# Optimization experiments

Hardware: AMD Instinct MI355X
Metric: run time of the kernel (lower is better)

Reference implementation:

```python
import jax, jax.numpy as jnp
import numpy as np

N = 100000   # n_nodes
E = 600000   # n_edges
D = 128      # cfg_node_encoding_dim
L = 4        # nr_layers
EPS = 1e-5


def setup_inputs() -> dict:
    key = jax.random.key(0)
    k0, k1, k2, k3 = jax.random.split(key, 4)
    x = jax.random.normal(k0, (N, D), dtype=jnp.float32)
    edge_index = jax.random.randint(k1, (2, E), 0, N, dtype=jnp.int32)
    W = jax.random.normal(k2, (L, D, D), dtype=jnp.float32) * (1.0 / np.sqrt(D))
    b = jax.random.normal(k3, (L, D), dtype=jnp.float32) * 0.01
    gamma = jnp.ones((L, D), dtype=jnp.float32)
    beta = jnp.zeros((L, D), dtype=jnp.float32)
    return {"x": x, "W": W, "b": b, "gamma": gamma, "beta": beta,
            "edge_index": edge_index}


def _gcn_layer(x, W, b, src_sl, dst_sl, norm):
    # PyG GCNConv: h = x @ W, then symmetric-normalized aggregation + bias
    h = x @ W                                  # [N, D]
    msg = h[src_sl] * norm[:, None]            # [E+N, D] gather + scale
    out = jax.ops.segment_sum(msg, dst_sl, num_segments=N)  # scatter-add
    return out + b


def _layer_norm(x, gamma, beta):
    mu = jnp.mean(x, axis=-1, keepdims=True)
    var = jnp.mean(jnp.square(x - mu), axis=-1, keepdims=True)
    return (x - mu) * jax.lax.rsqrt(var + EPS) * gamma + beta


def reference(x, W, b, gamma, beta, edge_index):
    src, dst = edge_index[0], edge_index[1]
    loops = jnp.arange(N, dtype=edge_index.dtype)
    src_sl = jnp.concatenate([src, loops])     # add_self_loops=True
    dst_sl = jnp.concatenate([dst, loops])
    deg = jax.ops.segment_sum(jnp.ones(E + N, dtype=x.dtype), dst_sl,
                              num_segments=N)
    dinv = jnp.where(deg > 0, jax.lax.rsqrt(deg), 0.0)
    norm = dinv[src_sl] * dinv[dst_sl]         # D^{-1/2} (A+I) D^{-1/2}
    h = x
    for i in range(L):
        h = _gcn_layer(h, W[i], b[i], src_sl, dst_sl, norm)
        h = jax.nn.relu(h)
        # dropout is identity in eval mode
        h = _layer_norm(h, gamma[i], beta[i])
    return h
```

## Files before the change

kernel.cpp:

```cpp
#include <hip/hip_runtime.h>
#include <hip/hip_bf16.h>

#define D_DIM 128
#define AST 136
#define CST 132

typedef __attribute__((ext_vector_type(8))) short short8v;
typedef __attribute__((ext_vector_type(4))) short short4v;
typedef __attribute__((ext_vector_type(4))) float floatx4;

__device__ __forceinline__ short f2bf(float x) {
    unsigned u = __builtin_bit_cast(unsigned, x);
    unsigned r = u + 0x7fff + ((u >> 16) & 1);
    return (short)(r >> 16);
}
__device__ __forceinline__ float bflo(unsigned p) {
    return __builtin_bit_cast(float, p << 16);
}
__device__ __forceinline__ float bfhi(unsigned p) {
    return __builtin_bit_cast(float, p & 0xffff0000u);
}


__global__ void zero_cnt_kernel(int* __restrict__ cnt, int n) {
    int i = blockIdx.x * blockDim.x + threadIdx.x;
    if (i < n) cnt[i] = 0;
}

__global__ void count_kernel(const int* __restrict__ dst, int* __restrict__ cnt, int e) {
    int i = blockIdx.x * blockDim.x + threadIdx.x;
    if (i < e) atomicAdd(&cnt[dst[i]], 1);
}

__global__ __launch_bounds__(256) void partial_kernel(const int* __restrict__ cnt,
                                                      int* __restrict__ partial, int n) {
    const int b = blockIdx.x, t = threadIdx.x;
    const int base = b * 1024 + t * 4;
    int s = 0;
    if (base + 3 < n) {
        int4 c = *(const int4*)(cnt + base);
        s = c.x + c.y + c.z + c.w;
    } else {
        for (int j = 0; j < 4; ++j) if (base + j < n) s += cnt[base + j];
    }
    #pragma unroll
    for (int m = 1; m < 64; m <<= 1) s += __shfl_xor(s, m, 64);
    __shared__ int ws[4];
    if ((t & 63) == 0) ws[t >> 6] = s;
    __syncthreads();
    if (t == 0) partial[b] = ws[0] + ws[1] + ws[2] + ws[3];
}

__global__ __launch_bounds__(1024) void scan_partials_kernel(int* __restrict__ partial, int nb,
                                                             int* __restrict__ row_ptr,
                                                             int n, int e) {
    __shared__ int sh[1024];
    const int t = threadIdx.x;
    sh[t] = (t < nb) ? partial[t] : 0;
    __syncthreads();
    for (int off = 1; off < 1024; off <<= 1) {
        int v = (t >= off) ? sh[t - off] : 0;
        __syncthreads();
        sh[t] += v;
        __syncthreads();
    }
    if (t < nb) partial[t] = (t == 0) ? 0 : sh[t - 1];
    if (t == 0) row_ptr[n] = e;
}

__global__ __launch_bounds__(256) void emit_kernel(const int* __restrict__ cnt,
                                                   const int* __restrict__ partial,
                                                   int* __restrict__ row_ptr,
                                                   int* __restrict__ cursor,
                                                   float* __restrict__ dinv, int n) {
    const int b = blockIdx.x, t = threadIdx.x;
    const int base = b * 1024 + t * 4;
    int4 c = make_int4(0, 0, 0, 0);
    if (base + 3 < n) {
        c = *(const int4*)(cnt + base);
    } else {
        if (base     < n) c.x = cnt[base];
        if (base + 1 < n) c.y = cnt[base + 1];
        if (base + 2 < n) c.z = cnt[base + 2];
        if (base + 3 < n) c.w = cnt[base + 3];
    }
    const int ts = c.x + c.y + c.z + c.w;
    int incl = ts;
    const int lane = t & 63;
    #pragma unroll
    for (int off = 1; off < 64; off <<= 1) {
        int v = __shfl_up(incl, off, 64);
        if (lane >= off) incl += v;
    }
    __shared__ int wsum[4];
    if (lane == 63) wsum[t >> 6] = incl;
    __syncthreads();
    const int w = t >> 6;
    int waveoff = 0;
    #pragma unroll
    for (int i = 0; i < 3; ++i) if (i < w) waveoff += wsum[i];
    const int basev = partial[b] + waveoff + (incl - ts);
    const int e0 = basev, e1 = e0 + c.x, e2 = e1 + c.y, e3 = e2 + c.z;
    if (base + 3 < n) {
        *(int4*)(row_ptr + base) = make_int4(e0, e1, e2, e3);
        *(int4*)(cursor  + base) = make_int4(e0, e1, e2, e3);
        *(float4*)(dinv + base) = make_float4(rsqrtf((float)(c.x + 1)), rsqrtf((float)(c.y + 1)),
                                              rsqrtf((float)(c.z + 1)), rsqrtf((float)(c.w + 1)));
    } else {
        int es[4] = {e0, e1, e2, e3};
        int cs[4] = {c.x, c.y, c.z, c.w};
        for (int j = 0; j < 4; ++j) if (base + j < n) {
            row_ptr[base + j] = es[j];
            cursor[base + j]  = es[j];
            dinv[base + j]    = rsqrtf((float)(cs[j] + 1));
        }
    }
}

__global__ void fill_kernel(const int* __restrict__ src, const int* __restrict__ dst,
                            const float* __restrict__ dinv,
                            int* __restrict__ cursor, int2* __restrict__ meta, int e) {
    int i = blockIdx.x * blockDim.x + threadIdx.x;
    if (i < e) {
        int s = src[i], d = dst[i];
        int p = atomicAdd(&cursor[d], 1);
        float w = dinv[s] * dinv[d];
        meta[p] = make_int2(s, __builtin_bit_cast(int, w));
    }
}

__global__ __launch_bounds__(256) void wt_prep_kernel(const float* __restrict__ W,
                                                      short* __restrict__ Wt, int total) {
    int o = blockIdx.x * blockDim.x + threadIdx.x;
    if (o >= total) return;
    int l = o >> 14;
    int r = o & 16383;
    int nn = r >> 7;
    int k  = r & 127;
    Wt[o] = f2bf(W[(size_t)l * 16384 + (size_t)k * 128 + nn]);
}

template <bool IN_F32>
__global__ __launch_bounds__(256) void gemm_mfma_kernel(const void* __restrict__ Xv,
                                                        const short* __restrict__ Wt,
                                                        short* __restrict__ H, int n) {
    __shared__ short Alds[64 * AST];
    const int t    = threadIdx.x;
    const int wv   = t >> 6;
    const int lane = t & 63;
    const int m    = lane & 15;
    const int quad = lane >> 4;
    const int row0 = blockIdx.x * 64;

    short8v bfr[2][4];
    #pragma unroll
    for (int c = 0; c < 2; ++c) {
        const short* bp = Wt + (size_t)((wv * 2 + c) * 16 + m) * D_DIM + quad * 8;
        #pragma unroll
        for (int kt = 0; kt < 4; ++kt)
            bfr[c][kt] = *(const short8v*)(bp + kt * 32);
    }

    if constexpr (IN_F32) {
        const float* X = (const float*)Xv;
        #pragma unroll
        for (int i = 0; i < 8; ++i) {
            int q  = t + i * 256;
            int r  = q >> 5;
            int k4 = q & 31;
            int row = row0 + r;
            float4 v = make_float4(0.f, 0.f, 0.f, 0.f);
            if (row < n) v = *(const float4*)(X + (size_t)row * D_DIM + k4 * 4);
            short4v s;
            s.x = f2bf(v.x); s.y = f2bf(v.y); s.z = f2bf(v.z); s.w = f2bf(v.w);
            *(short4v*)(&Alds[r * AST + k4 * 4]) = s;
        }
    } else {
        const short* X = (const short*)Xv;
        #pragma unroll
        for (int i = 0; i < 4; ++i) {
            int q  = t + i * 256;
            int r  = q >> 4;
            int kc = q & 15;
            int row = row0 + r;
            short8v v = {0,0,0,0,0,0,0,0};
            if (row < n) v = *(const short8v*)(X + (size_t)row * D_DIM + kc * 8);
            *(short8v*)(&Alds[r * AST + kc * 8]) = v;
        }
    }
    __syncthreads();

    floatx4 acc[4][2];
    #pragma unroll
    for (int rt = 0; rt < 4; ++rt) {
        const short* ab = &Alds[(rt * 16 + m) * AST + quad * 8];
        short8v afr[4];
        #pragma unroll
        for (int kt = 0; kt < 4; ++kt) afr[kt] = *(const short8v*)(ab + kt * 32);

        #pragma unroll
        for (int c = 0; c < 2; ++c) {
            floatx4 a = (floatx4){0.f, 0.f, 0.f, 0.f};
            #pragma unroll
            for (int kt = 0; kt < 4; ++kt)
                a = __builtin_amdgcn_mfma_f32_16x16x32_bf16(afr[kt], bfr[c][kt], a, 0, 0, 0);
            acc[rt][c] = a;
        }
    }
    __syncthreads();

    #pragma unroll
    for (int rt = 0; rt < 4; ++rt) {
        #pragma unroll
        for (int c = 0; c < 2; ++c) {
            const int col = (wv * 2 + c) * 16 + m;
            #pragma unroll
            for (int r = 0; r < 4; ++r)
                Alds[(rt * 16 + quad * 4 + r) * CST + col] = f2bf(acc[rt][c][r]);
        }
    }
    __syncthreads();

    #pragma unroll
    for (int i = 0; i < 4; ++i) {
        int q  = t + i * 256;
        int r  = q >> 4;
        int kc = q & 15;
        int row = row0 + r;
        if (row < n)
            *(short8v*)(H + (size_t)row * D_DIM + kc * 8) = *(const short8v*)(&Alds[r * CST + kc * 8]);
    }
}

template <bool OUT_BF16>
__global__ __launch_bounds__(256) void agg_kernel(const short* __restrict__ Hb,
                                                  const int* __restrict__ row_ptr,
                                                  const int2* __restrict__ meta,
                                                  const float* __restrict__ dinv,
                                                  const float* __restrict__ bias,
                                                  const float* __restrict__ gamma,
                                                  const float* __restrict__ beta,
                                                  void* __restrict__ Yv, int n) {
    const int wave = __builtin_amdgcn_readfirstlane(threadIdx.x >> 6);
    const int lane = threadIdx.x & 63;
    const int vA = (blockIdx.x * 4 + wave) * 2;
    if (vA >= n) return;
    const bool hasB = (vA + 1) < n;
    const int vB = hasB ? vA + 1 : vA;

    const float dvA = dinv[vA];
    const float dvB = dinv[vB];
    const int begA = row_ptr[vA];
    const int endA = row_ptr[vA + 1];
    const int begB = row_ptr[vB];
    const int endB = row_ptr[vB + 1];
    const int cntA = endA - begA;
    const int cntB = hasB ? (endB - begB) : 0;
    const int mx = cntA > cntB ? cntA : cntB;

    const unsigned psA = ((const unsigned*)(Hb + (size_t)vA * D_DIM))[lane];
    const unsigned psB = ((const unsigned*)(Hb + (size_t)vB * D_DIM))[lane];
    float axA = bflo(psA) * (dvA * dvA);
    float ayA = bfhi(psA) * (dvA * dvA);
    float axB = bflo(psB) * (dvB * dvB);
    float ayB = bfhi(psB) * (dvB * dvB);

    for (int k = 0; k < mx; k += 4) {
        int   idx[8];
        float wgt[8];
        #pragma unroll
        for (int j = 0; j < 4; ++j) {
            int ii = min(begA + k + j, endA - 1); ii = max(ii, 0);
            const int2 mm = meta[ii];
            idx[j] = mm.x;
            wgt[j] = (k + j < cntA) ? __builtin_bit_cast(float, mm.y) : 0.f;
        }
        #pragma unroll
        for (int j = 0; j < 4; ++j) {
            int ii = min(begB + k + j, endB - 1); ii = max(ii, 0);
            const int2 mm = meta[ii];
            idx[4 + j] = mm.x;
            wgt[4 + j] = (k + j < cntB) ? __builtin_bit_cast(float, mm.y) : 0.f;
        }
        unsigned p[8];
        #pragma unroll
        for (int j = 0; j < 8; ++j)
            p[j] = ((const unsigned*)(Hb + (size_t)idx[j] * D_DIM))[lane];
        #pragma unroll
        for (int j = 0; j < 4; ++j) {
            axA = fmaf(wgt[j], bflo(p[j]), axA);
            ayA = fmaf(wgt[j], bfhi(p[j]), ayA);
            axB = fmaf(wgt[4 + j], bflo(p[4 + j]), axB);
            ayB = fmaf(wgt[4 + j], bfhi(p[4 + j]), ayB);
        }
    }

    const float2 bb = ((const float2*)bias)[lane];
    const float2 gg = ((const float2*)gamma)[lane];
    const float2 be = ((const float2*)beta)[lane];

    #pragma unroll
    for (int s = 0; s < 2; ++s) {
        if (s == 1 && !hasB) break;
        float a0 = fmaxf((s ? axB : axA) + bb.x, 0.f);
        float a1 = fmaxf((s ? ayB : ayA) + bb.y, 0.f);
        float s1 = a0 + a1;
        float s2 = a0 * a0 + a1 * a1;
        #pragma unroll
        for (int m = 1; m < 64; m <<= 1) {
            s1 += __shfl_xor(s1, m, 64);
            s2 += __shfl_xor(s2, m, 64);
        }
        const float mu  = s1 * (1.f / 128.f);
        const float var = s2 * (1.f / 128.f) - mu * mu;
        const float rs  = rsqrtf(var + 1e-5f);
        const float o0 = (a0 - mu) * rs * gg.x + be.x;
        const float o1 = (a1 - mu) * rs * gg.y + be.y;
        const int v = s ? vB : vA;
        if constexpr (OUT_BF16) {
            unsigned pack = (unsigned)(unsigned short)f2bf(o0) |
                            ((unsigned)(unsigned short)f2bf(o1) << 16);
            ((unsigned*)((short*)Yv + (size_t)v * D_DIM))[lane] = pack;
        } else {
            float2 o; o.x = o0; o.y = o1;
            ((float2*)((float*)Yv + (size_t)v * D_DIM))[lane] = o;
        }
    }
}


extern "C" void kernel_launch(void* const* d_in, const int* in_sizes, int n_in,
                              void* d_out, int out_size, void* d_ws, size_t ws_size,
                              hipStream_t stream) {
    const float* x     = (const float*)d_in[0];
    const float* W     = (const float*)d_in[1];
    const float* bias  = (const float*)d_in[2];
    const float* gamma = (const float*)d_in[3];
    const float* beta  = (const float*)d_in[4];
    const int*   edges = (const int*)d_in[5];

    const int N = in_sizes[0] / D_DIM;
    const int E = in_sizes[5] / 2;
    const int L = in_sizes[1] / (D_DIM * D_DIM);

    const int* src = edges;
    const int* dst = edges + E;

    const int NB = (N + 1023) / 1024;

    char* w = (char*)d_ws;
    short* Hb   = (short*)w; w += (size_t)N * D_DIM * sizeof(short);
    short* Act  = (short*)w; w += (size_t)N * D_DIM * sizeof(short);
    int* cnt     = (int*)w;  w += (size_t)((N + 3) & ~3) * sizeof(int);
    int* row_ptr = (int*)w;  w += (size_t)((N + 4) & ~3) * sizeof(int);
    int* cursor  = (int*)w;  w += (size_t)((N + 3) & ~3) * sizeof(int);
    int2* meta   = (int2*)w; w += (size_t)E * sizeof(int2);
    float* dinv  = (float*)w; w += (size_t)((N + 3) & ~3) * sizeof(float);
    int* partial = (int*)w;  w += (size_t)((NB + 3) & ~3) * sizeof(int);
    short* Wt    = (short*)w; w += (size_t)L * D_DIM * D_DIM * sizeof(short);

    zero_cnt_kernel<<<(N + 255) / 256, 256, 0, stream>>>(cnt, N);
    count_kernel<<<(E + 255) / 256, 256, 0, stream>>>(dst, cnt, E);
    partial_kernel<<<NB, 256, 0, stream>>>(cnt, partial, N);
    scan_partials_kernel<<<1, 1024, 0, stream>>>(partial, NB, row_ptr, N, E);
    emit_kernel<<<NB, 256, 0, stream>>>(cnt, partial, row_ptr, cursor, dinv, N);
    fill_kernel<<<(E + 255) / 256, 256, 0, stream>>>(src, dst, dinv, cursor, meta, E);

    const int WT_TOTAL = L * D_DIM * D_DIM;
    wt_prep_kernel<<<(WT_TOTAL + 255) / 256, 256, 0, stream>>>(W, Wt, WT_TOTAL);

    const int GB = (N + 63) / 64;
    const int AB = (N + 7) / 8;

    gemm_mfma_kernel<true><<<GB, 256, 0, stream>>>(x, Wt, Hb, N);
    agg_kernel<true><<<AB, 256, 0, stream>>>(Hb, row_ptr, meta, dinv,
                                             bias, gamma, beta, Act, N);
    for (int l = 1; l < L - 1; ++l) {
        gemm_mfma_kernel<false><<<GB, 256, 0, stream>>>(Act, Wt + (size_t)l * D_DIM * D_DIM, Hb, N);
        agg_kernel<true><<<AB, 256, 0, stream>>>(Hb, row_ptr, meta, dinv,
                                                 bias + (size_t)l * D_DIM,
                                                 gamma + (size_t)l * D_DIM,
                                                 beta + (size_t)l * D_DIM, Act, N);
    }
    {
        int l = L - 1;
        gemm_mfma_kernel<false><<<GB, 256, 0, stream>>>(Act, Wt + (size_t)l * D_DIM * D_DIM, Hb, N);
        agg_kernel<false><<<AB, 256, 0, stream>>>(Hb, row_ptr, meta, dinv,
                                                  bias + (size_t)l * D_DIM,
                                                  gamma + (size_t)l * D_DIM,
                                                  beta + (size_t)l * D_DIM, d_out, N);
    }
}
```

Before: 370.4 us.

## Add padded 16-slot per-node neighbor table for fixed-width aggregation gathers

Builds a padded per-node table of up to 16 (src, weight) records, initialised to weight zero, alongside the CSR meta array. The aggregation kernel loads both nodes' slots with one coalesced wave load, broadcasts indices through readlane, and issues 32 row gathers without per-edge bounds logic. It falls back to the CSR loop only for nodes with more than 16 edges. This costs an extra 12.8 MB table plus an init kernel, and wastes gather bandwidth on padding slots, since average degree is about 6.

```diff
diff --git a/kernel.cpp b/kernel.cpp
--- a/kernel.cpp
+++ b/kernel.cpp
@@ -25,6 +25,11 @@
 __global__ void zero_cnt_kernel(int* __restrict__ cnt, int n) {
     int i = blockIdx.x * blockDim.x + threadIdx.x;
     if (i < n) cnt[i] = 0;
+}
+
+__global__ void packed_init_kernel(int2* __restrict__ packed, int n16) {
+    int i = blockIdx.x * blockDim.x + threadIdx.x;
+    if (i < n16) packed[i] = make_int2(i >> 4, 0);
 }
 
 __global__ void count_kernel(const int* __restrict__ dst, int* __restrict__ cnt, int e) {
@@ -119,13 +124,18 @@
 
 __global__ void fill_kernel(const int* __restrict__ src, const int* __restrict__ dst,
                             const float* __restrict__ dinv,
-                            int* __restrict__ cursor, int2* __restrict__ meta, int e) {
+                            const int* __restrict__ row_ptr,
+                            int* __restrict__ cursor, int2* __restrict__ meta,
+                            int2* __restrict__ packed, int e) {
     int i = blockIdx.x * blockDim.x + threadIdx.x;
     if (i < e) {
         int s = src[i], d = dst[i];
         int p = atomicAdd(&cursor[d], 1);
         float w = dinv[s] * dinv[d];
-        meta[p] = make_int2(s, __builtin_bit_cast(int, w));
+        int2 rec = make_int2(s, __builtin_bit_cast(int, w));
+        meta[p] = rec;
+        int j = p - row_ptr[d];
+        if (j < 16) packed[(size_t)d * 16 + j] = rec;
     }
 }
 
@@ -234,6 +244,8 @@
 
 template <bool OUT_BF16>
 __global__ __launch_bounds__(256) void agg_kernel(const short* __restrict__ Hb,
+                                                  const int2* __restrict__ packed,
+                                                  const int* __restrict__ cnt,
                                                   const int* __restrict__ row_ptr,
                                                   const int2* __restrict__ meta,
                                                   const float* __restrict__ dinv,
@@ -248,56 +260,88 @@
     const bool hasB = (vA + 1) < n;
     const int vB = hasB ? vA + 1 : vA;
 
-    const float dvA = dinv[vA];
-    const float dvB = dinv[vB];
-    const int begA = row_ptr[vA];
-    const int endA = row_ptr[vA + 1];
-    const int begB = row_ptr[vB];
-    const int endB = row_ptr[vB + 1];
-    const int cntA = endA - begA;
-    const int cntB = hasB ? (endB - begB) : 0;
-    const int mx = cntA > cntB ? cntA : cntB;
-
+    const int2   cc  = *(const int2*)(cnt + vA);
+    const float2 dv2 = *(const float2*)(dinv + vA);
+    const float2 bb  = ((const float2*)bias)[lane];
+    const float2 gg  = ((const float2*)gamma)[lane];
+    const float2 be  = ((const float2*)beta)[lane];
+    const int2 mm = packed[(size_t)vA * 16 + (lane & 31)];
     const unsigned psA = ((const unsigned*)(Hb + (size_t)vA * D_DIM))[lane];
     const unsigned psB = ((const unsigned*)(Hb + (size_t)vB * D_DIM))[lane];
+
+    const float dvA = dv2.x;
+    const float dvB = hasB ? dv2.y : dv2.x;
+
     float axA = bflo(psA) * (dvA * dvA);
     float ayA = bfhi(psA) * (dvA * dvA);
     float axB = bflo(psB) * (dvB * dvB);
     float ayB = bfhi(psB) * (dvB * dvB);
 
-    for (int k = 0; k < mx; k += 4) {
-        int   idx[8];
-        float wgt[8];
-        #pragma unroll
-        for (int j = 0; j < 4; ++j) {
-            int ii = min(begA + k + j, endA - 1); ii = max(ii, 0);
-            const int2 mm = meta[ii];
-            idx[j] = mm.x;
-            wgt[j] = (k + j < cntA) ? __builtin_bit_cast(float, mm.y) : 0.f;
-        }
-        #pragma unroll
-        for (int j = 0; j < 4; ++j) {
-            int ii = min(begB + k + j, endB - 1); ii = max(ii, 0);
-            const int2 mm = meta[ii];
-            idx[4 + j] = mm.x;
-            wgt[4 + j] = (k + j < cntB) ? __builtin_bit_cast(float, mm.y) : 0.f;
-        }
-        unsigned p[8];
-        #pragma unroll
-        for (int j = 0; j < 8; ++j)
-            p[j] = ((const unsigned*)(Hb + (size_t)idx[j] * D_DIM))[lane];
-        #pragma unroll
-        for (int j = 0; j < 4; ++j) {
-            axA = fmaf(wgt[j], bflo(p[j]), axA);
-            ayA = fmaf(wgt[j], bfhi(p[j]), ayA);
-            axB = fmaf(wgt[4 + j], bflo(p[4 + j]), axB);
-            ayB = fmaf(wgt[4 + j], bfhi(p[4 + j]), ayB);
-        }
-    }
-
-    const float2 bb = ((const float2*)bias)[lane];
-    const float2 gg = ((const float2*)gamma)[lane];
-    const float2 be = ((const float2*)beta)[lane];
+    unsigned p[32];
+    #pragma unroll
+    for (int j = 0; j < 16; ++j) {
+        const int s = __builtin_amdgcn_readlane(mm.x, j);
+        p[j] = ((const unsigned*)(Hb + (size_t)s * D_DIM))[lane];
+    }
+    if (hasB) {
+        #pragma unroll
+        for (int j = 0; j < 16; ++j) {
+            const int s = __builtin_amdgcn_readlane(mm.x, 16 + j);
+            p[16 + j] = ((const unsigned*)(Hb + (size_t)s * D_DIM))[lane];
+        }
+    } else {
+        #pragma unroll
+        for (int j = 0; j < 16; ++j) p[16 + j] = 0u;
+    }
+
+    #pragma unroll
+    for (int j = 0; j < 16; ++j) {
+        const float wA = __builtin_bit_cast(float, __builtin_amdgcn_readlane(mm.y, j));
+        const float wB = hasB ? __builtin_bit_cast(float, __builtin_amdgcn_readlane(mm.y, 16 + j)) : 0.f;
+        axA = fmaf(wA, bflo(p[j]), axA);
+        ayA = fmaf(wA, bfhi(p[j]), ayA);
+        axB = fmaf(wB, bflo(p[16 + j]), axB);
+        ayB = fmaf(wB, bfhi(p[16 + j]), ayB);
+    }
+
+    const int cntA = cc.x;
+    const int cntB = hasB ? cc.y : 0;
+    if ((cntA > 16) | (cntB > 16)) {
+        const int begA = __builtin_amdgcn_readfirstlane(row_ptr[vA]);
+        const int endA = begA + cntA;
+        const int begB = __builtin_amdgcn_readfirstlane(row_ptr[vB]);
+        const int endB = begB + cntB;
+        const int mx = cntA > cntB ? cntA : cntB;
+        for (int k = 16; k < mx; k += 4) {
+            int   idx[8];
+            float wgt[8];
+            #pragma unroll
+            for (int j = 0; j < 4; ++j) {
+                int ii = min(begA + k + j, endA - 1); ii = max(ii, begA);
+                const int2 m2 = meta[ii];
+                idx[j] = m2.x;
+                wgt[j] = (k + j < cntA) ? __builtin_bit_cast(float, m2.y) : 0.f;
+            }
+            #pragma unroll
+            for (int j = 0; j < 4; ++j) {
+                int ii = min(begB + k + j, endB - 1); ii = max(ii, begB);
+                const int2 m2 = meta[ii];
+                idx[4 + j] = m2.x;
+                wgt[4 + j] = (k + j < cntB) ? __builtin_bit_cast(float, m2.y) : 0.f;
+            }
+            unsigned q[8];
+            #pragma unroll
+            for (int j = 0; j < 8; ++j)
+                q[j] = ((const unsigned*)(Hb + (size_t)idx[j] * D_DIM))[lane];
+            #pragma unroll
+            for (int j = 0; j < 4; ++j) {
+                axA = fmaf(wgt[j], bflo(q[j]), axA);
+                ayA = fmaf(wgt[j], bfhi(q[j]), ayA);
+                axB = fmaf(wgt[4 + j], bflo(q[4 + j]), axB);
+                ayB = fmaf(wgt[4 + j], bfhi(q[4 + j]), ayB);
+            }
+        }
+    }
 
     #pragma unroll
     for (int s = 0; s < 2; ++s) {
@@ -349,22 +393,25 @@
     const int NB = (N + 1023) / 1024;
 
     char* w = (char*)d_ws;
-    short* Hb   = (short*)w; w += (size_t)N * D_DIM * sizeof(short);
-    short* Act  = (short*)w; w += (size_t)N * D_DIM * sizeof(short);
+    short* Hb    = (short*)w; w += (size_t)N * D_DIM * sizeof(short);
+    short* Act   = (short*)w; w += (size_t)N * D_DIM * sizeof(short);
     int* cnt     = (int*)w;  w += (size_t)((N + 3) & ~3) * sizeof(int);
     int* row_ptr = (int*)w;  w += (size_t)((N + 4) & ~3) * sizeof(int);
     int* cursor  = (int*)w;  w += (size_t)((N + 3) & ~3) * sizeof(int);
     int2* meta   = (int2*)w; w += (size_t)E * sizeof(int2);
+    int2* packed = (int2*)w; w += (size_t)N * 16 * sizeof(int2);
     float* dinv  = (float*)w; w += (size_t)((N + 3) & ~3) * sizeof(float);
     int* partial = (int*)w;  w += (size_t)((NB + 3) & ~3) * sizeof(int);
     short* Wt    = (short*)w; w += (size_t)L * D_DIM * D_DIM * sizeof(short);
 
     zero_cnt_kernel<<<(N + 255) / 256, 256, 0, stream>>>(cnt, N);
+    packed_init_kernel<<<(N * 16 + 255) / 256, 256, 0, stream>>>(packed, N * 16);
     count_kernel<<<(E + 255) / 256, 256, 0, stream>>>(dst, cnt, E);
     partial_kernel<<<NB, 256, 0, stream>>>(cnt, partial, N);
     scan_partials_kernel<<<1, 1024, 0, stream>>>(partial, NB, row_ptr, N, E);
     emit_kernel<<<NB, 256, 0, stream>>>(cnt, partial, row_ptr, cursor, dinv, N);
-    fill_kernel<<<(E + 255) / 256, 256, 0, stream>>>(src, dst, dinv, cursor, meta, E);
+    fill_kernel<<<(E + 255) / 256, 256, 0, stream>>>(src, dst, dinv, row_ptr,
+                                                     cursor, meta, packed, E);
 
     const int WT_TOTAL = L * D_DIM * D_DIM;
     wt_prep_kernel<<<(WT_TOTAL + 255) / 256, 256, 0, stream>>>(W, Wt, WT_TOTAL);
@@ -373,11 +420,11 @@
     const int AB = (N + 7) / 8;
 
     gemm_mfma_kernel<true><<<GB, 256, 0, stream>>>(x, Wt, Hb, N);
-    agg_kernel<true><<<AB, 256, 0, stream>>>(Hb, row_ptr, meta, dinv,
+    agg_kernel<true><<<AB, 256, 0, stream>>>(Hb, packed, cnt, row_ptr, meta, dinv,
                                              bias, gamma, beta, Act, N);
     for (int l = 1; l < L - 1; ++l) {
         gemm_mfma_kernel<false><<<GB, 256, 0, stream>>>(Act, Wt + (size_t)l * D_DIM * D_DIM, Hb, N);
-        agg_kernel<true><<<AB, 256, 0, stream>>>(Hb, row_ptr, meta, dinv,
+        agg_kernel<true><<<AB, 256, 0, stream>>>(Hb, packed, cnt, row_ptr, meta, dinv,
                                                  bias + (size_t)l * D_DIM,
                                                  gamma + (size_t)l * D_DIM,
                                                  beta + (size_t)l * D_DIM, Act, N);
@@ -385,7 +432,7 @@
     {
         int l = L - 1;
         gemm_mfma_kernel<false><<<GB, 256, 0, stream>>>(Act, Wt + (size_t)l * D_DIM * D_DIM, Hb, N);
-        agg_kernel<false><<<AB, 256, 0, stream>>>(Hb, row_ptr, meta, dinv,
+        agg_kernel<false><<<AB, 256, 0, stream>>>(Hb, packed, cnt, row_ptr, meta, dinv,
                                                   bias + (size_t)l * D_DIM,
                                                   gamma + (size_t)l * D_DIM,
                                                   beta + (size_t)l * D_DIM, d_out, N);
```

Measured after the change: 386.4 us. 4.3% more time.

## Replace CSR build with fixed-width padded adjacency plus overflow list

Applied to the files above, without the earlier changes.

Replaces the count/scan/emit/fill CSR construction with a padded 16-slot-per-node neighbor table filled by one atomic pass. Edges past 16 go to a global overflow list. The aggregation kernel reads a node's neighbor indices with one vector load and readlane, applies the dinv[src] weight on the fly, and folds dinv[dst] into the epilogue. This removes several small launches and the per-edge meta array. The cost is that nodes with more than 16 in-edges trigger a linear scan of the whole overflow list, and neighbor order becomes nondeterministic.

```diff
diff --git a/kernel.cpp b/kernel.cpp
--- a/kernel.cpp
+++ b/kernel.cpp
@@ -22,111 +22,35 @@
 }
 
 
-__global__ void zero_cnt_kernel(int* __restrict__ cnt, int n) {
+__global__ __launch_bounds__(256) void init_kernel(int* __restrict__ deg,
+                                                   int* __restrict__ packedi,
+                                                   int* __restrict__ ovcnt, int n16) {
     int i = blockIdx.x * blockDim.x + threadIdx.x;
-    if (i < n) cnt[i] = 0;
-}
-
-__global__ void count_kernel(const int* __restrict__ dst, int* __restrict__ cnt, int e) {
+    if (i < n16) {
+        packedi[i] = i >> 4;
+        if ((i & 15) == 0) deg[i >> 4] = 0;
+    }
+    if (i == 0) *ovcnt = 0;
+}
+
+__global__ void fill2_kernel(const int* __restrict__ src, const int* __restrict__ dst,
+                             int* __restrict__ deg, int* __restrict__ packedi,
+                             int2* __restrict__ ov, int* __restrict__ ovcnt, int e) {
     int i = blockIdx.x * blockDim.x + threadIdx.x;
-    if (i < e) atomicAdd(&cnt[dst[i]], 1);
-}
-
-__global__ __launch_bounds__(256) void partial_kernel(const int* __restrict__ cnt,
-                                                      int* __restrict__ partial, int n) {
-    const int b = blockIdx.x, t = threadIdx.x;
-    const int base = b * 1024 + t * 4;
-    int s = 0;
-    if (base + 3 < n) {
-        int4 c = *(const int4*)(cnt + base);
-        s = c.x + c.y + c.z + c.w;
+    if (i >= e) return;
+    int s = src[i], d = dst[i];
+    int j = atomicAdd(&deg[d], 1);
+    if (j < 16) {
+        packedi[(size_t)d * 16 + j] = s;
     } else {
-        for (int j = 0; j < 4; ++j) if (base + j < n) s += cnt[base + j];
-    }
-    #pragma unroll
-    for (int m = 1; m < 64; m <<= 1) s += __shfl_xor(s, m, 64);
-    __shared__ int ws[4];
-    if ((t & 63) == 0) ws[t >> 6] = s;
-    __syncthreads();
-    if (t == 0) partial[b] = ws[0] + ws[1] + ws[2] + ws[3];
-}
-
-__global__ __launch_bounds__(1024) void scan_partials_kernel(int* __restrict__ partial, int nb,
-                                                             int* __restrict__ row_ptr,
-                                                             int n, int e) {
-    __shared__ int sh[1024];
-    const int t = threadIdx.x;
-    sh[t] = (t < nb) ? partial[t] : 0;
-    __syncthreads();
-    for (int off = 1; off < 1024; off <<= 1) {
-        int v = (t >= off) ? sh[t - off] : 0;
-        __syncthreads();
-        sh[t] += v;
-        __syncthreads();
-    }
-    if (t < nb) partial[t] = (t == 0) ? 0 : sh[t - 1];
-    if (t == 0) row_ptr[n] = e;
-}
-
-__global__ __launch_bounds__(256) void emit_kernel(const int* __restrict__ cnt,
-                                                   const int* __restrict__ partial,
-                                                   int* __restrict__ row_ptr,
-                                                   int* __restrict__ cursor,
-                                                   float* __restrict__ dinv, int n) {
-    const int b = blockIdx.x, t = threadIdx.x;
-    const int base = b * 1024 + t * 4;
-    int4 c = make_int4(0, 0, 0, 0);
-    if (base + 3 < n) {
-        c = *(const int4*)(cnt + base);
-    } else {
-        if (base     < n) c.x = cnt[base];
-        if (base + 1 < n) c.y = cnt[base + 1];
-        if (base + 2 < n) c.z = cnt[base + 2];
-        if (base + 3 < n) c.w = cnt[base + 3];
-    }
-    const int ts = c.x + c.y + c.z + c.w;
-    int incl = ts;
-    const int lane = t & 63;
-    #pragma unroll
-    for (int off = 1; off < 64; off <<= 1) {
-        int v = __shfl_up(incl, off, 64);
-        if (lane >= off) incl += v;
-    }
-    __shared__ int wsum[4];
-    if (lane == 63) wsum[t >> 6] = incl;
-    __syncthreads();
-    const int w = t >> 6;
-    int waveoff = 0;
-    #pragma unroll
-    for (int i = 0; i < 3; ++i) if (i < w) waveoff += wsum[i];
-    const int basev = partial[b] + waveoff + (incl - ts);
-    const int e0 = basev, e1 = e0 + c.x, e2 = e1 + c.y, e3 = e2 + c.z;
-    if (base + 3 < n) {
-        *(int4*)(row_ptr + base) = make_int4(e0, e1, e2, e3);
-        *(int4*)(cursor  + base) = make_int4(e0, e1, e2, e3);
-        *(float4*)(dinv + base) = make_float4(rsqrtf((float)(c.x + 1)), rsqrtf((float)(c.y + 1)),
-                                              rsqrtf((float)(c.z + 1)), rsqrtf((float)(c.w + 1)));
-    } else {
-        int es[4] = {e0, e1, e2, e3};
-        int cs[4] = {c.x, c.y, c.z, c.w};
-        for (int j = 0; j < 4; ++j) if (base + j < n) {
-            row_ptr[base + j] = es[j];
-            cursor[base + j]  = es[j];
-            dinv[base + j]    = rsqrtf((float)(cs[j] + 1));
-        }
-    }
-}
-
-__global__ void fill_kernel(const int* __restrict__ src, const int* __restrict__ dst,
-                            const float* __restrict__ dinv,
-                            int* __restrict__ cursor, int2* __restrict__ meta, int e) {
+        int k = atomicAdd(ovcnt, 1);
+        ov[k] = make_int2(d, s);
+    }
+}
+
+__global__ void dinv_kernel(const int* __restrict__ deg, float* __restrict__ dinv, int n) {
     int i = blockIdx.x * blockDim.x + threadIdx.x;
-    if (i < e) {
-        int s = src[i], d = dst[i];
-        int p = atomicAdd(&cursor[d], 1);
-        float w = dinv[s] * dinv[d];
-        meta[p] = make_int2(s, __builtin_bit_cast(int, w));
-    }
+    if (i < n) dinv[i] = rsqrtf((float)deg[i] + 1.0f);
 }
 
 __global__ __launch_bounds__(256) void wt_prep_kernel(const float* __restrict__ W,
@@ -234,9 +158,11 @@
 
 template <bool OUT_BF16>
 __global__ __launch_bounds__(256) void agg_kernel(const short* __restrict__ Hb,
-                                                  const int* __restrict__ row_ptr,
-                                                  const int2* __restrict__ meta,
+                                                  const int* __restrict__ packedi,
+                                                  const int* __restrict__ deg,
                                                   const float* __restrict__ dinv,
+                                                  const int2* __restrict__ ov,
+                                                  const int* __restrict__ ovcnt,
                                                   const float* __restrict__ bias,
                                                   const float* __restrict__ gamma,
                                                   const float* __restrict__ beta,
@@ -248,62 +174,102 @@
     const bool hasB = (vA + 1) < n;
     const int vB = hasB ? vA + 1 : vA;
 
+    const int cntA = deg[vA];
+    const int cntB = hasB ? deg[vB] : 0;
     const float dvA = dinv[vA];
     const float dvB = dinv[vB];
-    const int begA = row_ptr[vA];
-    const int endA = row_ptr[vA + 1];
-    const int begB = row_ptr[vB];
-    const int endB = row_ptr[vB + 1];
-    const int cntA = endA - begA;
-    const int cntB = hasB ? (endB - begB) : 0;
-    const int mx = cntA > cntB ? cntA : cntB;
-
-    const unsigned psA = ((const unsigned*)(Hb + (size_t)vA * D_DIM))[lane];
-    const unsigned psB = ((const unsigned*)(Hb + (size_t)vB * D_DIM))[lane];
-    float axA = bflo(psA) * (dvA * dvA);
-    float ayA = bfhi(psA) * (dvA * dvA);
-    float axB = bflo(psB) * (dvB * dvB);
-    float ayB = bfhi(psB) * (dvB * dvB);
-
-    for (int k = 0; k < mx; k += 4) {
-        int   idx[8];
-        float wgt[8];
-        #pragma unroll
-        for (int j = 0; j < 4; ++j) {
-            int ii = min(begA + k + j, endA - 1); ii = max(ii, 0);
-            const int2 mm = meta[ii];
-            idx[j] = mm.x;
-            wgt[j] = (k + j < cntA) ? __builtin_bit_cast(float, mm.y) : 0.f;
-        }
-        #pragma unroll
-        for (int j = 0; j < 4; ++j) {
-            int ii = min(begB + k + j, endB - 1); ii = max(ii, 0);
-            const int2 mm = meta[ii];
-            idx[4 + j] = mm.x;
-            wgt[4 + j] = (k + j < cntB) ? __builtin_bit_cast(float, mm.y) : 0.f;
-        }
-        unsigned p[8];
-        #pragma unroll
-        for (int j = 0; j < 8; ++j)
-            p[j] = ((const unsigned*)(Hb + (size_t)idx[j] * D_DIM))[lane];
-        #pragma unroll
-        for (int j = 0; j < 4; ++j) {
-            axA = fmaf(wgt[j], bflo(p[j]), axA);
-            ayA = fmaf(wgt[j], bfhi(p[j]), ayA);
-            axB = fmaf(wgt[4 + j], bflo(p[4 + j]), axB);
-            ayB = fmaf(wgt[4 + j], bfhi(p[4 + j]), ayB);
-        }
-    }
-
+
+    const int sl = lane & 31;
+    const int pk = packedi[(size_t)vA * 16 + (hasB ? sl : (sl & 15))];
     const float2 bb = ((const float2*)bias)[lane];
     const float2 gg = ((const float2*)gamma)[lane];
     const float2 be = ((const float2*)beta)[lane];
+    const unsigned psA = ((const unsigned*)(Hb + (size_t)vA * D_DIM))[lane];
+    const unsigned psB = ((const unsigned*)(Hb + (size_t)vB * D_DIM))[lane];
+
+    float axA = bflo(psA) * dvA;
+    float ayA = bfhi(psA) * dvA;
+    float axB = bflo(psB) * dvB;
+    float ayB = bfhi(psB) * dvB;
+
+    unsigned p[16];
+    float    w[16];
+    #pragma unroll
+    for (int j = 0; j < 8; ++j) {
+        const int sA = __builtin_amdgcn_readlane(pk, j);
+        const int sB = __builtin_amdgcn_readlane(pk, 16 + j);
+        p[j]     = ((const unsigned*)(Hb + (size_t)sA * D_DIM))[lane];
+        p[8 + j] = ((const unsigned*)(Hb + (size_t)sB * D_DIM))[lane];
+        w[j]     = (j < cntA) ? dinv[sA] : 0.f;
+        w[8 + j] = (j < cntB) ? dinv[sB] : 0.f;
+    }
+    #pragma unroll
+    for (int j = 0; j < 8; ++j) {
+        axA = fmaf(w[j], bflo(p[j]), axA);
+        ayA = fmaf(w[j], bfhi(p[j]), ayA);
+        axB = fmaf(w[8 + j], bflo(p[8 + j]), axB);
+        ayB = fmaf(w[8 + j], bfhi(p[8 + j]), ayB);
+    }
+    if ((cntA > 8) | (cntB > 8)) {
+        #pragma unroll
+        for (int j = 0; j < 4; ++j) {
+            const int sA = __builtin_amdgcn_readlane(pk, 8 + j);
+            const int sB = __builtin_amdgcn_readlane(pk, 24 + j);
+            p[j]     = ((const unsigned*)(Hb + (size_t)sA * D_DIM))[lane];
+            p[4 + j] = ((const unsigned*)(Hb + (size_t)sB * D_DIM))[lane];
+            w[j]     = (8 + j < cntA) ? dinv[sA] : 0.f;
+            w[4 + j] = (8 + j < cntB) ? dinv[sB] : 0.f;
+        }
+        #pragma unroll
+        for (int j = 0; j < 4; ++j) {
+            axA = fmaf(w[j], bflo(p[j]), axA);
+            ayA = fmaf(w[j], bfhi(p[j]), ayA);
+            axB = fmaf(w[4 + j], bflo(p[4 + j]), axB);
+            ayB = fmaf(w[4 + j], bfhi(p[4 + j]), ayB);
+        }
+        if ((cntA > 12) | (cntB > 12)) {
+            #pragma unroll
+            for (int j = 0; j < 4; ++j) {
+                const int sA = __builtin_amdgcn_readlane(pk, 12 + j);
+                const int sB = __builtin_amdgcn_readlane(pk, 28 + j);
+                p[j]     = ((const unsigned*)(Hb + (size_t)sA * D_DIM))[lane];
+                p[4 + j] = ((const unsigned*)(Hb + (size_t)sB * D_DIM))[lane];
+                w[j]     = (12 + j < cntA) ? dinv[sA] : 0.f;
+                w[4 + j] = (12 + j < cntB) ? dinv[sB] : 0.f;
+            }
+            #pragma unroll
+            for (int j = 0; j < 4; ++j) {
+                axA = fmaf(w[j], bflo(p[j]), axA);
+                ayA = fmaf(w[j], bfhi(p[j]), ayA);
+                axB = fmaf(w[4 + j], bflo(p[4 + j]), axB);
+                ayB = fmaf(w[4 + j], bfhi(p[4 + j]), ayB);
+            }
+        }
+        if ((cntA > 16) | (cntB > 16)) {
+            const int oc = *ovcnt;
+            for (int k = 0; k < oc; ++k) {
+                const int2 eo = ov[k];
+                if ((eo.x == vA) | (eo.x == vB)) {
+                    const float ws = dinv[eo.y];
+                    const unsigned q = ((const unsigned*)(Hb + (size_t)eo.y * D_DIM))[lane];
+                    if (eo.x == vA) {
+                        axA = fmaf(ws, bflo(q), axA);
+                        ayA = fmaf(ws, bfhi(q), ayA);
+                    } else {
+                        axB = fmaf(ws, bflo(q), axB);
+                        ayB = fmaf(ws, bfhi(q), ayB);
+                    }
+                }
+            }
+        }
+    }
 
     #pragma unroll
     for (int s = 0; s < 2; ++s) {
         if (s == 1 && !hasB) break;
-        float a0 = fmaxf((s ? axB : axA) + bb.x, 0.f);
-        float a1 = fmaxf((s ? ayB : ayA) + bb.y, 0.f);
+        const float dv = s ? dvB : dvA;
+        float a0 = fmaxf(fmaf(dv, (s ? axB : axA), bb.x), 0.f);
+        float a1 = fmaxf(fmaf(dv, (s ? ayB : ayA), bb.y), 0.f);
         float s1 = a0 + a1;
         float s2 = a0 * a0 + a1 * a1;
         #pragma unroll
@@ -346,25 +312,19 @@
     const int* src = edges;
     const int* dst = edges + E;
 
-    const int NB = (N + 1023) / 1024;
-
     char* w = (char*)d_ws;
-    short* Hb   = (short*)w; w += (size_t)N * D_DIM * sizeof(short);
-    short* Act  = (short*)w; w += (size_t)N * D_DIM * sizeof(short);
-    int* cnt     = (int*)w;  w += (size_t)((N + 3) & ~3) * sizeof(int);
-    int* row_ptr = (int*)w;  w += (size_t)((N + 4) & ~3) * sizeof(int);
-    int* cursor  = (int*)w;  w += (size_t)((N + 3) & ~3) * sizeof(int);
-    int2* meta   = (int2*)w; w += (size_t)E * sizeof(int2);
-    float* dinv  = (float*)w; w += (size_t)((N + 3) & ~3) * sizeof(float);
-    int* partial = (int*)w;  w += (size_t)((NB + 3) & ~3) * sizeof(int);
-    short* Wt    = (short*)w; w += (size_t)L * D_DIM * D_DIM * sizeof(short);
-
-    zero_cnt_kernel<<<(N + 255) / 256, 256, 0, stream>>>(cnt, N);
-    count_kernel<<<(E + 255) / 256, 256, 0, stream>>>(dst, cnt, E);
-    partial_kernel<<<NB, 256, 0, stream>>>(cnt, partial, N);
-    scan_partials_kernel<<<1, 1024, 0, stream>>>(partial, NB, row_ptr, N, E);
-    emit_kernel<<<NB, 256, 0, stream>>>(cnt, partial, row_ptr, cursor, dinv, N);
-    fill_kernel<<<(E + 255) / 256, 256, 0, stream>>>(src, dst, dinv, cursor, meta, E);
+    short* Hb      = (short*)w; w += (size_t)N * D_DIM * sizeof(short);
+    short* Act     = (short*)w; w += (size_t)N * D_DIM * sizeof(short);
+    int*   deg     = (int*)w;   w += (size_t)((N + 3) & ~3) * sizeof(int);
+    int*   packedi = (int*)w;   w += (size_t)N * 16 * sizeof(int);
+    float* dinv    = (float*)w; w += (size_t)((N + 3) & ~3) * sizeof(float);
+    int2*  ov      = (int2*)w;  w += (size_t)E * sizeof(int2);
+    int*   ovcnt   = (int*)w;   w += 16;
+    short* Wt      = (short*)w; w += (size_t)L * D_DIM * D_DIM * sizeof(short);
+
+    init_kernel<<<(N * 16 + 255) / 256, 256, 0, stream>>>(deg, packedi, ovcnt, N * 16);
+    fill2_kernel<<<(E + 255) / 256, 256, 0, stream>>>(src, dst, deg, packedi, ov, ovcnt, E);
+    dinv_kernel<<<(N + 255) / 256, 256, 0, stream>>>(deg, dinv, N);
 
     const int WT_TOTAL = L * D_DIM * D_DIM;
     wt_prep_kernel<<<(WT_TOTAL + 255) / 256, 256, 0, stream>>>(W, Wt, WT_TOTAL);
@@ -373,11 +333,11 @@
     const int AB = (N + 7) / 8;
 
     gemm_mfma_kernel<true><<<GB, 256, 0, stream>>>(x, Wt, Hb, N);
-    agg_kernel<true><<<AB, 256, 0, stream>>>(Hb, row_ptr, meta, dinv,
+    agg_kernel<true><<<AB, 256, 0, stream>>>(Hb, packedi, deg, dinv, ov, ovcnt,
                                              bias, gamma, beta, Act, N);
     for (int l = 1; l < L - 1; ++l) {
         gemm_mfma_kernel<false><<<GB, 256, 0, stream>>>(Act, Wt + (size_t)l * D_DIM * D_DIM, Hb, N);
-        agg_kernel<true><<<AB, 256, 0, stream>>>(Hb, row_ptr, meta, dinv,
+        agg_kernel<true><<<AB, 256, 0, stream>>>(Hb, packedi, deg, dinv, ov, ovcnt,
                                                  bias + (size_t)l * D_DIM,
                                                  gamma + (size_t)l * D_DIM,
                                                  beta + (size_t)l * D_DIM, Act, N);
@@ -385,7 +345,7 @@
     {
         int l = L - 1;
         gemm_mfma_kernel<false><<<GB, 256, 0, stream>>>(Act, Wt + (size_t)l * D_DIM * D_DIM, Hb, N);
-        agg_kernel<false><<<AB, 256, 0, stream>>>(Hb, row_ptr, meta, dinv,
+        agg_kernel<false><<<AB, 256, 0, stream>>>(Hb, packedi, deg, dinv, ov, ovcnt,
                                                   bias + (size_t)l * D_DIM,
                                                   gamma + (size_t)l * D_DIM,
                                                   beta + (size_t)l * D_DIM, d_out, N);
```

Result: faster. 341.3 us (-7.9%).
